# Kernel tuning notes

Hardware: AMD Instinct MI355X
Metric: run time of the kernel (lower is better)

The kernel has to match this reference:

```python
import jax, jax.numpy as jnp
import numpy as np

ALPHA = 0.9

def setup_inputs() -> dict:
    key = jax.random.key(0)
    k1, k2 = jax.random.split(key)
    x = jax.random.normal(k1, (1024, 32, 1024), dtype=jnp.float32)
    state = jax.random.normal(k2, (32, 1024), dtype=jnp.float32)
    return {"x": x, "state": state}

def reference(x, state):
    # EMA recurrence: s_t = alpha * s_{t-1} + (1 - alpha) * x_t
    def step(s, xt):
        s = xt * (1.0 - ALPHA) + s * ALPHA
        return s, s
    final_state, out = jax.lax.scan(step, state, x)
    return out, final_state
```

## Files before the change

kernel.cpp:

```cpp
#include <hip/hip_runtime.h>


constexpr int T = 1024;
constexpr int C = 32 * 1024;
constexpr int CHUNK = 256;
constexpr int NCHUNK = T / CHUNK;
constexpr int WARM = 128;

__global__ __launch_bounds__(256)
void ExponentialDecay_23708219474744_kernel(const float* __restrict__ x,
                                            const float* __restrict__ state,
                                            float* __restrict__ out) {
    const int ch = blockIdx.x * blockDim.x + threadIdx.x;
    const int chunk = blockIdx.y;
    const int t0 = chunk * CHUNK;

    const float a = 0.9f;
    const float oma = 0.1f;

    float s;
    if (chunk == 0) {
        s = state[ch];
    } else {
        s = 0.0f;
        const int tw = t0 - WARM;
        #pragma unroll 8
        for (int t = tw; t < t0; ++t) {
            float xv = x[(size_t)t * C + ch];
            s = fmaf(s, a, xv * oma);
        }
    }

    const int t1 = t0 + CHUNK;
    #pragma unroll 8
    for (int t = t0; t < t1; ++t) {
        float xv = x[(size_t)t * C + ch];
        s = fmaf(s, a, xv * oma);
        out[(size_t)t * C + ch] = s;
    }

    if (chunk == NCHUNK - 1) {
        out[(size_t)T * C + ch] = s;
    }
}

extern "C" void kernel_launch(void* const* d_in, const int* in_sizes, int n_in,
                              void* d_out, int out_size, void* d_ws, size_t ws_size,
                              hipStream_t stream) {
    const float* x = (const float*)d_in[0];
    const float* state = (const float*)d_in[1];
    float* out = (float*)d_out;

    dim3 block(256);
    dim3 grid(C / 256, NCHUNK);
    ExponentialDecay_23708219474744_kernel<<<grid, block, 0, stream>>>(x, state, out);
}
```

Baseline: 244.8 us.

## Vectorize EMA scan to float4 with register double-buffered loads and smaller chunks

Each thread now handles four channels through 128-bit loads and stores. It prefetches the next group of eight timesteps into registers while computing the current group, and writes output with nontemporal stores. Chunk size and warm-up length drop to 64, which raises the block count in the time dimension from 4 to 16 while shrinking the grid along channels by a factor of four. The warm-up re-read overhead becomes relatively larger. The shorter warm-up (0.9^64 ≈ 1e-3) also loosens accuracy for the carried-in state.

```diff
diff --git a/kernel.cpp b/kernel.cpp
--- a/kernel.cpp
+++ b/kernel.cpp
@@ -1,57 +1,94 @@
 #include <hip/hip_runtime.h>
 
 
+typedef float f32x4 __attribute__((ext_vector_type(4)));
+
 constexpr int T = 1024;
 constexpr int C = 32 * 1024;
-constexpr int CHUNK = 256;
+constexpr int CV = C / 4;
+constexpr int CHUNK = 64;
 constexpr int NCHUNK = T / CHUNK;
-constexpr int WARM = 128;
+constexpr int WARM = 64;
+constexpr int G = 8;
 
 __global__ __launch_bounds__(256)
-void ExponentialDecay_23708219474744_kernel(const float* __restrict__ x,
-                                            const float* __restrict__ state,
-                                            float* __restrict__ out) {
-    const int ch = blockIdx.x * blockDim.x + threadIdx.x;
+void ExponentialDecay_23708219474744_kernel(const f32x4* __restrict__ x4,
+                                            const f32x4* __restrict__ state4,
+                                            f32x4* __restrict__ out4) {
+    const int cv = blockIdx.x * blockDim.x + threadIdx.x;
     const int chunk = blockIdx.y;
     const int t0 = chunk * CHUNK;
-
     const float a = 0.9f;
     const float oma = 0.1f;
 
-    float s;
+    f32x4 s = {};
+    int tb;
     if (chunk == 0) {
-        s = state[ch];
+        s = state4[cv];
+        tb = 0;
     } else {
-        s = 0.0f;
-        const int tw = t0 - WARM;
-        #pragma unroll 8
-        for (int t = tw; t < t0; ++t) {
-            float xv = x[(size_t)t * C + ch];
-            s = fmaf(s, a, xv * oma);
+        tb = t0 - WARM;
+    }
+
+    const int nit = (chunk == 0) ? CHUNK : (CHUNK + WARM);
+    const int ng = nit / G;
+    const int gstore = (t0 - tb) / G;
+
+    const f32x4* __restrict__ xp = x4 + (size_t)tb * CV + cv;
+    f32x4* __restrict__ op = out4 + (size_t)t0 * CV + cv;
+
+    f32x4 cur[G], nxt[G];
+    #pragma unroll
+    for (int i = 0; i < G; ++i) cur[i] = xp[(size_t)i * CV];
+
+    for (int g = 0; g < ng; ++g) {
+        if (g + 1 < ng) {
+            const f32x4* __restrict__ xn = xp + (size_t)(g + 1) * G * CV;
+            #pragma unroll
+            for (int i = 0; i < G; ++i) nxt[i] = xn[(size_t)i * CV];
+        }
+
+        if (g >= gstore) {
+            f32x4* o = op + (size_t)(g - gstore) * G * CV;
+            #pragma unroll
+            for (int i = 0; i < G; ++i) {
+                f32x4 v = cur[i];
+                s.x = fmaf(s.x, a, v.x * oma);
+                s.y = fmaf(s.y, a, v.y * oma);
+                s.z = fmaf(s.z, a, v.z * oma);
+                s.w = fmaf(s.w, a, v.w * oma);
+                __builtin_nontemporal_store(s, o + (size_t)i * CV);
+            }
+        } else {
+            #pragma unroll
+            for (int i = 0; i < G; ++i) {
+                f32x4 v = cur[i];
+                s.x = fmaf(s.x, a, v.x * oma);
+                s.y = fmaf(s.y, a, v.y * oma);
+                s.z = fmaf(s.z, a, v.z * oma);
+                s.w = fmaf(s.w, a, v.w * oma);
+            }
+        }
+
+        if (g + 1 < ng) {
+            #pragma unroll
+            for (int i = 0; i < G; ++i) cur[i] = nxt[i];
         }
     }
 
-    const int t1 = t0 + CHUNK;
-    #pragma unroll 8
-    for (int t = t0; t < t1; ++t) {
-        float xv = x[(size_t)t * C + ch];
-        s = fmaf(s, a, xv * oma);
-        out[(size_t)t * C + ch] = s;
-    }
-
     if (chunk == NCHUNK - 1) {
-        out[(size_t)T * C + ch] = s;
+        out4[(size_t)T * CV + cv] = s;
     }
 }
 
 extern "C" void kernel_launch(void* const* d_in, const int* in_sizes, int n_in,
                               void* d_out, int out_size, void* d_ws, size_t ws_size,
                               hipStream_t stream) {
-    const float* x = (const float*)d_in[0];
-    const float* state = (const float*)d_in[1];
-    float* out = (float*)d_out;
+    const f32x4* x = (const f32x4*)d_in[0];
+    const f32x4* state = (const f32x4*)d_in[1];
+    f32x4* out = (f32x4*)d_out;
 
     dim3 block(256);
-    dim3 grid(C / 256, NCHUNK);
+    dim3 grid(CV / 256, NCHUNK);
     ExponentialDecay_23708219474744_kernel<<<grid, block, 0, stream>>>(x, state, out);
 }
```

New measurement: 254.9 us. +4.1%, slower.
